# Optimization experiments

Hardware: AMD Instinct MI355X
Metric: run time of the kernel (lower is better)

Reference implementation:

```python
import jax, jax.numpy as jnp
import numpy as np

QMIN, QMAX = 0.0, 255.0  # uint8 affine quantization range


def _quant_dequant(x, scale, zero_point):
    # affine static quantization: q = clamp(round(x/scale) + zp, 0, 255)
    q = jnp.clip(jnp.round(x / scale) + zero_point, QMIN, QMAX)
    # dequantize back to float for the reference GEMM
    return (q - zero_point) * scale


def setup_inputs() -> dict:
    key = jax.random.key(0)
    k1, k2, k3, k4, k5 = jax.random.split(key, 5)
    N, IN, OUT = 4096, 4096, 4096
    x = jax.random.normal(k1, (N, IN), dtype=jnp.float32)
    weight = jax.random.normal(k2, (OUT, IN), dtype=jnp.float32) * 0.02
    bias = jax.random.normal(k3, (OUT,), dtype=jnp.float32)
    # static qparams (as produced by calculate_qparams of the observers)
    act_scale = jnp.float32(4.0 * 2.0 / 255.0)  # covers ~[-4, 4]
    act_zero_point = jnp.int32(128)
    weight_scale = (jax.random.uniform(k4, (OUT,), dtype=jnp.float32) * 0.5 + 0.5) * (0.08 * 2.0 / 255.0)
    weight_zero_point = jnp.full((OUT,), 128, dtype=jnp.int32)
    return {
        "x": x,
        "weight": weight,
        "bias": bias,
        "act_scale": act_scale,
        "act_zero_point": act_zero_point,
        "weight_scale": weight_scale,
        "weight_zero_point": weight_zero_point,
    }


def reference(x, weight, bias, act_scale, act_zero_point, weight_scale, weight_zero_point):
    # per-tensor static activation quantization
    x_dq = _quant_dequant(x, act_scale, act_zero_point.astype(jnp.float32))  # [N, in]
    # per-output-row weight quantization (block_size = (1, in_features))
    w_dq = _quant_dequant(
        weight,
        weight_scale[:, None],
        weight_zero_point.astype(jnp.float32)[:, None],
    )  # [out, in]
    # F.linear: x @ W^T + b
    return jnp.einsum("ni,oi->no", x_dq, w_dq) + bias
```

## Files before the change

kernel.cpp:

```cpp
#include <hip/hip_runtime.h>
#include <stdint.h>

typedef int   int4v   __attribute__((ext_vector_type(4)));
typedef float float4v __attribute__((ext_vector_type(4)));

static constexpr int DIM = 4096;
static constexpr int BM  = 256, BN = 256;
static constexpr int BK  = 128;
static constexpr int NKT = DIM / BK;

__global__ __launch_bounds__(256) void quant_act_kernel(
    const float* __restrict__ x, const float* __restrict__ s_ptr,
    const int* __restrict__ zp_ptr, int* __restrict__ out, int n4) {
  const float s  = s_ptr[0];
  const int   zp = zp_ptr[0];
  int idx    = blockIdx.x * blockDim.x + threadIdx.x;
  int stride = gridDim.x * blockDim.x;
  for (int i = idx; i < n4; i += stride) {
    float4v v = reinterpret_cast<const float4v*>(x)[i];
    int packed = 0;
#pragma unroll
    for (int j = 0; j < 4; ++j) {
      int q = (int)rintf(v[j] / s) + zp;
      q = min(max(q, 0), 255);
      q -= zp;
      packed |= (q & 255) << (8 * j);
    }
    out[i] = packed;
  }
}

__global__ __launch_bounds__(256) void quant_wgt_kernel(
    const float* __restrict__ w, const float* __restrict__ ws,
    const int* __restrict__ wzp, int* __restrict__ out, int n4) {
  int idx    = blockIdx.x * blockDim.x + threadIdx.x;
  int stride = gridDim.x * blockDim.x;
  for (int i = idx; i < n4; i += stride) {
    const int row = i >> 10;
    const float s = ws[row];
    const int  zp = wzp[row];
    float4v v = reinterpret_cast<const float4v*>(w)[i];
    int packed = 0;
#pragma unroll
    for (int j = 0; j < 4; ++j) {
      int q = (int)rintf(v[j] / s) + zp;
      q = min(max(q, 0), 255);
      q -= zp;
      packed |= (q & 255) << (8 * j);
    }
    out[i] = packed;
  }
}


#define MFMA_QUAD(AF, MH, NL)                                                  \
  __builtin_amdgcn_s_setprio(1);                                               \
  _Pragma("unroll") for (int kk = 0; kk < 2; ++kk)                             \
  _Pragma("unroll") for (int m = 0; m < 4; ++m)                                \
  _Pragma("unroll") for (int n = 0; n < 2; ++n)                                \
      acc[(MH)*4 + m][(NL) + n] = __builtin_amdgcn_mfma_i32_16x16x64_i8(       \
          AF[m][kk], bf[(NL) + n][kk], acc[(MH)*4 + m][(NL) + n], 0, 0, 0);    \
  __builtin_amdgcn_s_setprio(0);

__global__ __launch_bounds__(512) void gemm_i8_pipe(
    const signed char* __restrict__ A, const signed char* __restrict__ B,
    const float* __restrict__ s_act, const float* __restrict__ w_scale,
    const float* __restrict__ bias, float* __restrict__ C) {
  extern __shared__ signed char smem[];

  const int tid  = threadIdx.x;
  const int w    = tid >> 6;
  const int lane = tid & 63;
  const int wr = w >> 2, wc = w & 3;
  const int l15 = lane & 15, lhi = lane >> 4;
  const int swk = (l15 & 7) << 4;

  const int srow = lane >> 3;
  const int scol = ((lane & 7) ^ (lane >> 3)) << 4;

  const int tileM = blockIdx.y * BM;
  const int tileN = blockIdx.x * BN;

  auto stageA = [&](int i, int ktn, signed char* aL) {
    const int c = 4 * w + i;
    const size_t g = (size_t)(tileM + c * 8 + srow) * DIM + (size_t)ktn * BK + scol;
    __builtin_amdgcn_global_load_lds(
        (const __attribute__((address_space(1))) void*)(A + g),
        (__attribute__((address_space(3))) void*)(aL + c * 1024), 16, 0, 0);
  };
  auto stageB = [&](int i, int ktn, signed char* bL) {
    const int c = 4 * w + i;
    const size_t g = (size_t)(tileN + c * 8 + srow) * DIM + (size_t)ktn * BK + scol;
    __builtin_amdgcn_global_load_lds(
        (const __attribute__((address_space(1))) void*)(B + g),
        (__attribute__((address_space(3))) void*)(bL + c * 1024), 16, 0, 0);
  };
  auto rdA = [&](const signed char* aL, int mh, int m, int kk) -> int4v {
    const int r = wr * 128 + (mh * 4 + m) * 16 + l15;
    return *(const int4v*)(aL + r * BK + ((kk * 64 + lhi * 16) ^ swk));
  };
  auto rdB = [&](const signed char* bL, int nidx, int kk) -> int4v {
    const int r = wc * 64 + nidx * 16 + l15;
    return *(const int4v*)(bL + r * BK + ((kk * 64 + lhi * 16) ^ swk));
  };

  int4v acc[8][4] = {};
  int4v afLo[4][2];
  int4v afHi[4][2];
  int4v bf[4][2];

  {
    signed char* a0 = smem;
    signed char* b0 = smem + 32768;
    signed char* a1 = smem + 65536;
    signed char* b1 = smem + 65536 + 32768;
#pragma unroll
    for (int i = 0; i < 4; ++i) { stageA(i, 0, a0); stageB(i, 0, b0); }
#pragma unroll
    for (int i = 0; i < 4; ++i) { stageA(i, 1, a1); stageB(i, 1, b1); }
    asm volatile("s_waitcnt vmcnt(8)" ::: "memory");
    __builtin_amdgcn_s_barrier();
#pragma unroll
    for (int m = 0; m < 4; ++m) { afLo[m][0] = rdA(a0, 0, m, 0); afLo[m][1] = rdA(a0, 0, m, 1); }
#pragma unroll
    for (int n = 0; n < 2; ++n) { bf[n][0] = rdB(b0, n, 0); bf[n][1] = rdB(b0, n, 1); }
  }

  for (int kt = 0; kt < NKT; ++kt) {
    signed char* aL = smem + (kt & 1) * 65536;
    signed char* bL = aL + 32768;
    signed char* aN = smem + ((kt + 1) & 1) * 65536;
    signed char* bN = aN + 32768;

#pragma unroll
    for (int n = 2; n < 4; ++n) { bf[n][0] = rdB(bL, n, 0); bf[n][1] = rdB(bL, n, 1); }
    MFMA_QUAD(afLo, 0, 0)

#pragma unroll
    for (int m = 0; m < 4; ++m) { afHi[m][0] = rdA(aL, 1, m, 0); afHi[m][1] = rdA(aL, 1, m, 1); }
    MFMA_QUAD(afLo, 0, 2)
    asm volatile("s_waitcnt lgkmcnt(0)" ::: "memory");
    __builtin_amdgcn_s_barrier();

    if (kt + 2 < NKT) {
#pragma unroll
      for (int i = 0; i < 4; ++i) { stageA(i, kt + 2, aL); stageB(i, kt + 2, bL); }
    }
    MFMA_QUAD(afHi, 1, 0)
    if (kt + 2 < NKT) {
      asm volatile("s_waitcnt vmcnt(8)" ::: "memory");
    } else {
      asm volatile("s_waitcnt vmcnt(0)" ::: "memory");
    }
    __builtin_amdgcn_s_barrier();

    if (kt + 1 < NKT) {
#pragma unroll
      for (int m = 0; m < 4; ++m) { afLo[m][0] = rdA(aN, 0, m, 0); afLo[m][1] = rdA(aN, 0, m, 1); }
#pragma unroll
      for (int n = 0; n < 2; ++n) { bf[n][0] = rdB(bN, n, 0); bf[n][1] = rdB(bN, n, 1); }
    }
    MFMA_QUAD(afHi, 1, 2)
  }

  const float sa = s_act[0];
#pragma unroll
  for (int n = 0; n < 4; ++n) {
    const int col = tileN + wc * 64 + n * 16 + l15;
    const float sc = sa * w_scale[col];
    const float bs = bias[col];
#pragma unroll
    for (int m = 0; m < 8; ++m) {
      const int rbase = tileM + wr * 128 + m * 16 + lhi * 4;
#pragma unroll
      for (int j = 0; j < 4; ++j)
        C[(size_t)(rbase + j) * DIM + col] = (float)acc[m][n][j] * sc + bs;
    }
  }
}

extern "C" void kernel_launch(void* const* d_in, const int* in_sizes, int n_in,
                              void* d_out, int out_size, void* d_ws, size_t ws_size,
                              hipStream_t stream) {
  const float* x    = (const float*)d_in[0];
  const float* w    = (const float*)d_in[1];
  const float* bias = (const float*)d_in[2];
  const float* a_s  = (const float*)d_in[3];
  const int*   a_zp = (const int*)d_in[4];
  const float* w_s  = (const float*)d_in[5];
  const int*   w_zp = (const int*)d_in[6];
  float* out = (float*)d_out;

  signed char* a8 = (signed char*)d_ws;
  signed char* b8 = a8 + (size_t)DIM * DIM;

  const int n4 = DIM * DIM / 4;
  quant_act_kernel<<<2048, 256, 0, stream>>>(x, a_s, a_zp, (int*)a8, n4);
  quant_wgt_kernel<<<2048, 256, 0, stream>>>(w, w_s, w_zp, (int*)b8, n4);

  (void)hipFuncSetAttribute((const void*)gemm_i8_pipe,
                            hipFuncAttributeMaxDynamicSharedMemorySize, 131072);
  dim3 grid(DIM / BN, DIM / BM);
  gemm_i8_pipe<<<grid, 512, 131072, stream>>>(a8, b8, a_s, w_s, bias, out);
}
```

Measured before the change: 94.74 us.

## Interleave global-to-LDS staging with MFMA quadrants in ping-pong schedule

```diff
diff --git a/kernel.cpp b/kernel.cpp
--- a/kernel.cpp
+++ b/kernel.cpp
@@ -62,7 +62,7 @@
           AF[m][kk], bf[(NL) + n][kk], acc[(MH)*4 + m][(NL) + n], 0, 0, 0);    \
   __builtin_amdgcn_s_setprio(0);
 
-__global__ __launch_bounds__(512) void gemm_i8_pipe(
+__global__ __launch_bounds__(512) void gemm_i8_m201(
     const signed char* __restrict__ A, const signed char* __restrict__ B,
     const float* __restrict__ s_act, const float* __restrict__ w_scale,
     const float* __restrict__ bias, float* __restrict__ C) {
@@ -81,19 +81,21 @@
   const int tileM = blockIdx.y * BM;
   const int tileN = blockIdx.x * BN;
 
-  auto stageA = [&](int i, int ktn, signed char* aL) {
+  auto stageA = [&](int i, int t) {
+    signed char* dst = smem + (t & 1) * 65536;
     const int c = 4 * w + i;
-    const size_t g = (size_t)(tileM + c * 8 + srow) * DIM + (size_t)ktn * BK + scol;
+    const size_t g = (size_t)(tileM + c * 8 + srow) * DIM + (size_t)t * BK + scol;
     __builtin_amdgcn_global_load_lds(
         (const __attribute__((address_space(1))) void*)(A + g),
-        (__attribute__((address_space(3))) void*)(aL + c * 1024), 16, 0, 0);
-  };
-  auto stageB = [&](int i, int ktn, signed char* bL) {
+        (__attribute__((address_space(3))) void*)(dst + c * 1024), 16, 0, 0);
+  };
+  auto stageB = [&](int i, int t) {
+    signed char* dst = smem + (t & 1) * 65536 + 32768;
     const int c = 4 * w + i;
-    const size_t g = (size_t)(tileN + c * 8 + srow) * DIM + (size_t)ktn * BK + scol;
+    const size_t g = (size_t)(tileN + c * 8 + srow) * DIM + (size_t)t * BK + scol;
     __builtin_amdgcn_global_load_lds(
         (const __attribute__((address_space(1))) void*)(B + g),
-        (__attribute__((address_space(3))) void*)(bL + c * 1024), 16, 0, 0);
+        (__attribute__((address_space(3))) void*)(dst + c * 1024), 16, 0, 0);
   };
   auto rdA = [&](const signed char* aL, int mh, int m, int kk) -> int4v {
     const int r = wr * 128 + (mh * 4 + m) * 16 + l15;
@@ -109,58 +111,52 @@
   int4v afHi[4][2];
   int4v bf[4][2];
 
-  {
-    signed char* a0 = smem;
-    signed char* b0 = smem + 32768;
-    signed char* a1 = smem + 65536;
-    signed char* b1 = smem + 65536 + 32768;
-#pragma unroll
-    for (int i = 0; i < 4; ++i) { stageA(i, 0, a0); stageB(i, 0, b0); }
-#pragma unroll
-    for (int i = 0; i < 4; ++i) { stageA(i, 1, a1); stageB(i, 1, b1); }
-    asm volatile("s_waitcnt vmcnt(8)" ::: "memory");
-    __builtin_amdgcn_s_barrier();
-#pragma unroll
-    for (int m = 0; m < 4; ++m) { afLo[m][0] = rdA(a0, 0, m, 0); afLo[m][1] = rdA(a0, 0, m, 1); }
-#pragma unroll
-    for (int n = 0; n < 2; ++n) { bf[n][0] = rdB(b0, n, 0); bf[n][1] = rdB(b0, n, 1); }
-  }
+#pragma unroll
+  for (int i = 0; i < 4; ++i) { stageA(i, 0); stageB(i, 0); }
+  stageA(0, 1); stageB(0, 1); stageA(1, 1); stageB(1, 1);
+  asm volatile("s_waitcnt vmcnt(4)" ::: "memory");
+  __builtin_amdgcn_s_barrier();
 
   for (int kt = 0; kt < NKT; ++kt) {
-    signed char* aL = smem + (kt & 1) * 65536;
-    signed char* bL = aL + 32768;
-    signed char* aN = smem + ((kt + 1) & 1) * 65536;
-    signed char* bN = aN + 32768;
-
-#pragma unroll
-    for (int n = 2; n < 4; ++n) { bf[n][0] = rdB(bL, n, 0); bf[n][1] = rdB(bL, n, 1); }
+    const signed char* aC = smem + (kt & 1) * 65536;
+    const signed char* bC = aC + 32768;
+    const bool s1 = (kt + 1 < NKT);
+    const bool s2 = (kt + 2 < NKT);
+
+#pragma unroll
+    for (int m = 0; m < 4; ++m) { afLo[m][0] = rdA(aC, 0, m, 0); afLo[m][1] = rdA(aC, 0, m, 1); }
+#pragma unroll
+    for (int n = 0; n < 2; ++n) { bf[n][0] = rdB(bC, n, 0); bf[n][1] = rdB(bC, n, 1); }
+    if (s1) { stageA(2, kt + 1); stageB(2, kt + 1); }
+    __builtin_amdgcn_s_barrier();
+    asm volatile("s_waitcnt lgkmcnt(0)" ::: "memory");
     MFMA_QUAD(afLo, 0, 0)
-
-#pragma unroll
-    for (int m = 0; m < 4; ++m) { afHi[m][0] = rdA(aL, 1, m, 0); afHi[m][1] = rdA(aL, 1, m, 1); }
+    __builtin_amdgcn_s_barrier();
+
+#pragma unroll
+    for (int m = 0; m < 4; ++m) { afHi[m][0] = rdA(aC, 1, m, 0); afHi[m][1] = rdA(aC, 1, m, 1); }
+#pragma unroll
+    for (int n = 2; n < 4; ++n) { bf[n][0] = rdB(bC, n, 0); bf[n][1] = rdB(bC, n, 1); }
+    if (s1) { stageA(3, kt + 1); stageB(3, kt + 1); }
+    __builtin_amdgcn_s_barrier();
+    asm volatile("s_waitcnt lgkmcnt(0)" ::: "memory");
     MFMA_QUAD(afLo, 0, 2)
-    asm volatile("s_waitcnt lgkmcnt(0)" ::: "memory");
-    __builtin_amdgcn_s_barrier();
-
-    if (kt + 2 < NKT) {
-#pragma unroll
-      for (int i = 0; i < 4; ++i) { stageA(i, kt + 2, aL); stageB(i, kt + 2, bL); }
-    }
+    __builtin_amdgcn_s_barrier();
+
+    if (s2) { stageA(0, kt + 2); stageB(0, kt + 2); }
+    __builtin_amdgcn_s_barrier();
     MFMA_QUAD(afHi, 1, 0)
-    if (kt + 2 < NKT) {
-      asm volatile("s_waitcnt vmcnt(8)" ::: "memory");
+    __builtin_amdgcn_s_barrier();
+
+    if (s2) { stageA(1, kt + 2); stageB(1, kt + 2); }
+    __builtin_amdgcn_s_barrier();
+    MFMA_QUAD(afHi, 1, 2)
+    if (s2) {
+      asm volatile("s_waitcnt vmcnt(4)" ::: "memory");
     } else {
       asm volatile("s_waitcnt vmcnt(0)" ::: "memory");
     }
     __builtin_amdgcn_s_barrier();
-
-    if (kt + 1 < NKT) {
-#pragma unroll
-      for (int m = 0; m < 4; ++m) { afLo[m][0] = rdA(aN, 0, m, 0); afLo[m][1] = rdA(aN, 0, m, 1); }
-#pragma unroll
-      for (int n = 0; n < 2; ++n) { bf[n][0] = rdB(bN, n, 0); bf[n][1] = rdB(bN, n, 1); }
-    }
-    MFMA_QUAD(afHi, 1, 2)
   }
 
   const float sa = s_act[0];
@@ -198,8 +194,8 @@
   quant_act_kernel<<<2048, 256, 0, stream>>>(x, a_s, a_zp, (int*)a8, n4);
   quant_wgt_kernel<<<2048, 256, 0, stream>>>(w, w_s, w_zp, (int*)b8, n4);
 
-  (void)hipFuncSetAttribute((const void*)gemm_i8_pipe,
+  (void)hipFuncSetAttribute((const void*)gemm_i8_m201,
                             hipFuncAttributeMaxDynamicSharedMemorySize, 131072);
   dim3 grid(DIM / BN, DIM / BM);
-  gemm_i8_pipe<<<grid, 512, 131072, stream>>>(a8, b8, a_s, w_s, bias, out);
-}
+  gemm_i8_m201<<<grid, 512, 131072, stream>>>(a8, b8, a_s, w_s, bias, out);
+}
```

New measurement: 98.25 us. +3.7%, slower.
